# Kernel tuning notes

Hardware: AMD Instinct MI355X
Metric: run time of the kernel (lower is better)

The kernel has to match this reference:

```python
import jax, jax.numpy as jnp
import numpy as np

N_WORDS, L, VOCAB, D = 8192, 24, 128, 512
H, DK = 8, 64  # n_head, d_v (=d_k)
N_NAMES, WORDS_PER_NAME = 2048, 4
N_CONCEPTS, NAMES_PER_CONCEPT = 256, 8


def setup_inputs() -> dict:
    key = jax.random.key(0)
    ks = jax.random.split(key, 9)
    s = 1.0 / np.sqrt(D).astype(np.float32)
    inputs = jax.random.randint(ks[0], (N_WORDS, L), 0, VOCAB)  # 0 = pad char
    n_words = jnp.full((N_NAMES,), WORDS_PER_NAME, dtype=jnp.int32)
    n_names = jnp.full((N_CONCEPTS,), NAMES_PER_CONCEPT, dtype=jnp.int32)
    return {
        "inputs": inputs,
        "n_words": n_words,
        "n_names": n_names,
        "emb": jax.random.normal(ks[1], (VOCAB, D), jnp.float32) * s,
        "Wq": jax.random.normal(ks[2], (D, H * DK), jnp.float32) * s,
        "Wk": jax.random.normal(ks[3], (D, H * DK), jnp.float32) * s,
        "Wv": jax.random.normal(ks[4], (D, H * DK), jnp.float32) * s,
        "Wo": jax.random.normal(ks[5], (H * DK, D), jnp.float32) * s,
        "W1": jax.random.normal(ks[6], (D, 512), jnp.float32) * s,
        "W2": jax.random.normal(ks[7], (512, 256), jnp.float32) * s,
    }


def reference(inputs, n_words, n_names, emb, Wq, Wk, Wv, Wo, W1, W2):
    N, Lq = inputs.shape
    pad = inputs == 0  # [N, L] padding mask (char id 0)

    # --- MHAEncoder: embedding + masked multi-head self-attention ---
    x = emb[inputs]  # [N, L, D]
    def split_heads(t):  # [N, L, H*DK] -> [N, H, L, DK]
        return t.reshape(N, Lq, H, DK).transpose(0, 2, 1, 3)
    q = split_heads(x @ Wq)
    k = split_heads(x @ Wk)
    v = split_heads(x @ Wv)
    scale = jnp.asarray(1.0 / np.sqrt(DK), x.dtype)
    scores = jnp.einsum('nhqd,nhkd->nhqk', q, k) * scale  # [N, H, L, L]
    scores = jnp.where(pad[:, None, None, :], jnp.asarray(-1e9, x.dtype), scores)
    attn = jax.nn.softmax(scores, axis=-1)
    o = jnp.einsum('nhqk,nhkd->nhqd', attn, v)
    word_ft = o.transpose(0, 2, 1, 3).reshape(N, Lq, H * DK) @ Wo  # [N, L, D]

    # --- masked mean pooling over chars: matmul(mask, word_ft)/mask.sum(-1) ---
    m = (~pad).astype(word_ft.dtype)  # [N, L]
    name_emb = jnp.einsum('nl,nld->nd', m, word_ft) / m.sum(-1, keepdims=True)  # [N, D]

    # --- split(n_words) + per-group mean == segment mean over word groups ---
    G = n_words.shape[0]
    seg = jnp.repeat(jnp.arange(G), n_words, total_repeat_length=N)
    name_ft = jax.ops.segment_sum(name_emb, seg, num_segments=G)
    name_ft = name_ft / n_words[:, None].astype(name_ft.dtype)  # [G, D]

    # --- small no-bias Tanh MLP ---
    h = jnp.tanh(name_ft @ W1)
    out = jnp.tanh(h @ W2)  # [G, 256]
    # final .split(n_names) is a view-only regrouping; return the packed array
    return out
```

## Files before the change

kernel.cpp:

```cpp
#include <hip/hip_runtime.h>
#include <math.h>

#define NWORDS 8192
#define LW     24
#define VOC    128
#define DIM    512
#define NH     8
#define DKH    64
#define GNAMES 2048
#define F2     256

#define S1_LEN 458752

#define GEMM_BODY(A_, B_, K_, N_, m0_, n0_, kbeg_, kchunk_)                         \
  __shared__ float As[2][16][68];                                                   \
  __shared__ float Bs[2][16][68];                                                   \
  const int t = threadIdx.x, tx = t & 15, ty = t >> 4;                              \
  float acc[4][4] = {};                                                             \
  float ra[4], rb[4];                                                               \
  _Pragma("unroll")                                                                 \
  for (int i = 0; i < 4; ++i) { int idx = t + 256 * i;                              \
    ra[i] = A_[(size_t)(m0_ + (idx >> 4)) * K_ + kbeg_ + (idx & 15)]; }             \
  _Pragma("unroll")                                                                 \
  for (int i = 0; i < 4; ++i) { int idx = t + 256 * i;                              \
    rb[i] = B_[(size_t)(kbeg_ + (idx >> 6)) * N_ + n0_ + (idx & 63)]; }             \
  _Pragma("unroll")                                                                 \
  for (int i = 0; i < 4; ++i) { int idx = t + 256 * i; As[0][idx & 15][idx >> 4] = ra[i]; } \
  _Pragma("unroll")                                                                 \
  for (int i = 0; i < 4; ++i) { int idx = t + 256 * i; Bs[0][idx >> 6][idx & 63] = rb[i]; } \
  __syncthreads();                                                                  \
  int buf = 0;                                                                      \
  for (int k0 = kbeg_; k0 < kbeg_ + kchunk_; k0 += 16) {                            \
    const bool more = (k0 + 16 < kbeg_ + kchunk_);                                  \
    if (more) {                                                                     \
      _Pragma("unroll")                                                             \
      for (int i = 0; i < 4; ++i) { int idx = t + 256 * i;                          \
        ra[i] = A_[(size_t)(m0_ + (idx >> 4)) * K_ + (k0 + 16) + (idx & 15)]; }     \
      _Pragma("unroll")                                                             \
      for (int i = 0; i < 4; ++i) { int idx = t + 256 * i;                          \
        rb[i] = B_[(size_t)(k0 + 16 + (idx >> 6)) * N_ + n0_ + (idx & 63)]; }       \
    }                                                                               \
    _Pragma("unroll")                                                               \
    for (int k = 0; k < 16; ++k) {                                                  \
      float a[4], b[4];                                                             \
      _Pragma("unroll")                                                             \
      for (int i = 0; i < 4; ++i) a[i] = As[buf][k][ty * 4 + i];                    \
      _Pragma("unroll")                                                             \
      for (int j = 0; j < 4; ++j) b[j] = Bs[buf][k][tx * 4 + j];                    \
      _Pragma("unroll")                                                             \
      for (int i = 0; i < 4; ++i)                                                   \
        _Pragma("unroll")                                                           \
        for (int j = 0; j < 4; ++j) acc[i][j] += a[i] * b[j];                       \
    }                                                                               \
    if (more) {                                                                     \
      _Pragma("unroll")                                                             \
      for (int i = 0; i < 4; ++i) { int idx = t + 256 * i; As[buf ^ 1][idx & 15][idx >> 4] = ra[i]; } \
      _Pragma("unroll")                                                             \
      for (int i = 0; i < 4; ++i) { int idx = t + 256 * i; Bs[buf ^ 1][idx >> 6][idx & 63] = rb[i]; } \
      __syncthreads();                                                              \
      buf ^= 1;                                                                     \
    }                                                                               \
  }

template<int NSPLIT>
__global__ __launch_bounds__(256) void k_stage1(const float* __restrict__ emb,
                                                const float* __restrict__ Wq,
                                                const float* __restrict__ Wk,
                                                const float* __restrict__ Wv,
                                                const float* __restrict__ Wo,
                                                const float* __restrict__ W1,
                                                float* __restrict__ P) {
  const int tid = blockIdx.x, s = blockIdx.y;
  const float *A, *B;
  int coff, m0, n0;
  if (tid < 48) {
    const int g = tid >> 4, mt = tid & 15;
    A = emb;
    B = (g == 0) ? Wq : ((g == 1) ? Wk : Wv);
    coff = g * 65536;
    m0 = (mt >> 3) * 64; n0 = (mt & 7) * 64;
  } else {
    const int id = tid - 48;
    A = Wo; B = W1; coff = 3 * 65536;
    m0 = (id >> 3) * 64; n0 = (id & 7) * 64;
  }
  const int kchunk = 512 / NSPLIT, kbeg = s * kchunk;
  GEMM_BODY(A, B, 512, 512, m0, n0, kbeg, kchunk)
  float* Cp = P + (size_t)s * S1_LEN + coff;
  #pragma unroll
  for (int i = 0; i < 4; ++i) {
    float4 v = make_float4(acc[i][0], acc[i][1], acc[i][2], acc[i][3]);
    *(float4*)&Cp[(size_t)(m0 + ty * 4 + i) * 512 + n0 + tx * 4] = v;
  }
}

__global__ __launch_bounds__(256) void k_gemm_ilv(const float* __restrict__ A,
                                                  const float* __restrict__ B,
                                                  float* __restrict__ P,
                                                  int kchunk) {
  const int m0 = blockIdx.y * 64, n0 = blockIdx.x * 64;
  const int kbeg = blockIdx.z * kchunk;
  const int sz = blockIdx.z;
  GEMM_BODY(A, B, 512, 512, m0, n0, kbeg, kchunk)
  float4* P4 = (float4*)P;
  #pragma unroll
  for (int i = 0; i < 4; ++i) {
    float4 v = make_float4(acc[i][0], acc[i][1], acc[i][2], acc[i][3]);
    P4[((size_t)(m0 + ty * 4 + i) * 128 + (n0 >> 2) + tx) * 4 + sz] = v;
  }
}

__global__ __launch_bounds__(256) void k_npool(const float* __restrict__ Wn,
                                               const float* __restrict__ EV,
                                               float* __restrict__ NP) {
  const int m0 = blockIdx.x * 64, h = blockIdx.y;
  const float* A2 = Wn + (size_t)m0 * 1024 + h * 128;
  const float* B2 = EV + h * 64;
  GEMM_BODY(A2, B2, 1024, 512, 0, 0, 0, 128)
  #pragma unroll
  for (int i = 0; i < 4; ++i) {
    float4 v = make_float4(acc[i][0], acc[i][1], acc[i][2], acc[i][3]);
    *(float4*)&NP[(size_t)(m0 + ty * 4 + i) * 512 + h * 64 + tx * 4] = v;
  }
}

__global__ __launch_bounds__(256) void k_gemm_tail(const float* __restrict__ P,
                                                   const float* __restrict__ B,
                                                   float* __restrict__ C,
                                                   int kchunk) {
  const int N = 256, K = 512;
  __shared__ float As[2][16][68];
  __shared__ float Bs[2][16][68];
  const int t = threadIdx.x, tx = t & 15, ty = t >> 4;
  const int m0 = blockIdx.y * 64, n0 = blockIdx.x * 64;
  const int kbeg = blockIdx.z * kchunk;
  const float4* P4 = (const float4*)P;
  const int am = t >> 2, ak = t & 3;
  float acc[4][4] = {};
  float4 ta;
  float rb[4];
#define TAIL_LOAD_A(kb)                                                   \
  {                                                                       \
    size_t b4 = ((size_t)(m0 + am) * 128 + ((kb) >> 2) + ak) * 4;         \
    float4 p0 = P4[b4 + 0], p1 = P4[b4 + 1], p2 = P4[b4 + 2], p3 = P4[b4 + 3]; \
    ta.x = tanhf(p0.x + p1.x + p2.x + p3.x);                              \
    ta.y = tanhf(p0.y + p1.y + p2.y + p3.y);                              \
    ta.z = tanhf(p0.z + p1.z + p2.z + p3.z);                              \
    ta.w = tanhf(p0.w + p1.w + p2.w + p3.w);                              \
  }
#define TAIL_LOAD_B(kb)                                                   \
  _Pragma("unroll")                                                       \
  for (int i = 0; i < 4; ++i) { int idx = t + 256 * i;                    \
    rb[i] = B[(size_t)((kb) + (idx >> 6)) * N + n0 + (idx & 63)]; }
#define TAIL_STORE(bb)                                                    \
  { int kk = ak * 4;                                                      \
    As[bb][kk + 0][am] = ta.x; As[bb][kk + 1][am] = ta.y;                 \
    As[bb][kk + 2][am] = ta.z; As[bb][kk + 3][am] = ta.w; }               \
  _Pragma("unroll")                                                       \
  for (int i = 0; i < 4; ++i) { int idx = t + 256 * i;                    \
    Bs[bb][idx >> 6][idx & 63] = rb[i]; }
  TAIL_LOAD_A(kbeg)
  TAIL_LOAD_B(kbeg)
  TAIL_STORE(0)
  __syncthreads();
  int buf = 0;
  for (int k0 = kbeg; k0 < kbeg + kchunk; k0 += 16) {
    const bool more = (k0 + 16 < kbeg + kchunk);
    if (more) { TAIL_LOAD_A(k0 + 16) TAIL_LOAD_B(k0 + 16) }
    #pragma unroll
    for (int k = 0; k < 16; ++k) {
      float a[4], b[4];
      #pragma unroll
      for (int i = 0; i < 4; ++i) a[i] = As[buf][k][ty * 4 + i];
      #pragma unroll
      for (int j = 0; j < 4; ++j) b[j] = Bs[buf][k][tx * 4 + j];
      #pragma unroll
      for (int i = 0; i < 4; ++i)
        #pragma unroll
        for (int j = 0; j < 4; ++j) acc[i][j] += a[i] * b[j];
    }
    if (more) { TAIL_STORE(buf ^ 1) __syncthreads(); buf ^= 1; }
  }
  float* Cp = C + (size_t)blockIdx.z * (GNAMES * F2);
  #pragma unroll
  for (int i = 0; i < 4; ++i) {
    float4 v = make_float4(acc[i][0], acc[i][1], acc[i][2], acc[i][3]);
    *(float4*)&Cp[(size_t)(m0 + ty * 4 + i) * N + n0 + tx * 4] = v;
  }
}

template<int ACT, int S>
__global__ __launch_bounds__(256) void k_reduce(const float* __restrict__ P,
                                                float* __restrict__ O,
                                                int len4, int stride4) {
  const int i = blockIdx.x * 256 + threadIdx.x;
  if (i >= len4) return;
  const float4* P4 = (const float4*)P;
  float4 a = P4[i];
  #pragma unroll
  for (int s = 1; s < S; ++s) {
    float4 b = P4[(size_t)s * stride4 + i];
    a.x += b.x; a.y += b.y; a.z += b.z; a.w += b.w;
  }
  if (ACT) { a.x = tanhf(a.x); a.y = tanhf(a.y); a.z = tanhf(a.z); a.w = tanhf(a.w); }
  ((float4*)O)[i] = a;
}

__global__ __launch_bounds__(128) void k_qk_tab(const float* __restrict__ EQ,
                                                const float* __restrict__ EK,
                                                float* __restrict__ etab) {
  const int c1 = blockIdx.x, h = blockIdx.y, c2 = threadIdx.x;
  __shared__ float qrow[DKH];
  if (threadIdx.x < DKH) qrow[threadIdx.x] = EQ[c1 * DIM + h * DKH + threadIdx.x];
  __syncthreads();
  const float* krow = EK + c2 * DIM + h * DKH;
  float acc = 0.f;
  #pragma unroll
  for (int d = 0; d < DKH; ++d) acc += qrow[d] * krow[d];
  float e = (c1 != 0 && c2 != 0) ? __expf(acc * 0.125f) : 0.f;
  etab[((size_t)c1 * VOC + c2) * NH + h] = e;
}

__global__ __launch_bounds__(256) void k_bins(const int* __restrict__ inputs,
                                              const int* __restrict__ nwords,
                                              const float* __restrict__ etab,
                                              float* __restrict__ Wn) {
  const int g = blockIdx.x, t = threadIdx.x;
  const int wv = t >> 6, l = t & 63;
  const int h = l & 7, qg = l >> 3;
  __shared__ float bins[VOC * NH];
  __shared__ int wred[4];
  __shared__ int sh_nwg;

  for (int i = t; i < VOC * NH; i += 256) bins[i] = 0.f;
  int partial = 0;
  for (int i = t; i < GNAMES; i += 256) {
    int v = nwords[i];
    partial += (i < g) ? v : 0;
    if (i == g) sh_nwg = v;
  }
  #pragma unroll
  for (int d = 1; d < 64; d <<= 1) partial += __shfl_xor(partial, d);
  if (l == 0) wred[wv] = partial;
  __syncthreads();
  const int nw = sh_nwg;
  const int o0 = wred[0] + wred[1] + wred[2] + wred[3];

  for (int wrel = wv; wrel < nw; wrel += 4) {
    const int wi = o0 + wrel;
    int c_l = (l < LW) ? inputs[(size_t)wi * LW + l] : 0;
    unsigned long long mk = __ballot(c_l != 0);
    int cnt = __popcll(mk);
    float invc = cnt ? 1.f / (float)cnt : 0.f;

    int cq0 = __shfl(c_l, qg);
    int cq1 = __shfl(c_l, qg + 8);
    int cq2 = __shfl(c_l, qg + 16);
    const float* b0 = etab + (cq0 << 10) + h;
    const float* b1 = etab + (cq1 << 10) + h;
    const float* b2 = etab + (cq2 << 10) + h;

    float r0[LW], r1[LW], r2[LW];
    float d0 = 0.f, d1 = 0.f, d2 = 0.f;
    #pragma unroll
    for (int kp = 0; kp < LW; ++kp) {
      int o = __shfl(c_l, kp) << 3;
      r0[kp] = b0[o]; r1[kp] = b1[o]; r2[kp] = b2[o];
      d0 += r0[kp]; d1 += r1[kp]; d2 += r2[kp];
    }
    float i0 = cq0 ? invc / d0 : 0.f;
    float i1 = cq1 ? invc / d1 : 0.f;
    float i2 = cq2 ? invc / d2 : 0.f;

    #pragma unroll
    for (int kp = 0; kp < LW; ++kp) {
      int ck = __shfl(c_l, kp);
      if (ck) {
        float v = r0[kp] * i0 + r1[kp] * i1 + r2[kp] * i2;
        v += __shfl_xor(v, 8);
        v += __shfl_xor(v, 16);
        v += __shfl_xor(v, 32);
        if (qg == 0) atomicAdd(&bins[(ck << 3) + h], v);
      }
    }
  }
  __syncthreads();

  const float invn = nw ? 1.f / (float)nw : 0.f;
  for (int i = t; i < NH * VOC; i += 256) {
    int hh = i >> 7, cc = i & 127;
    Wn[(size_t)g * 1024 + i] = bins[(cc << 3) + hh] * invn;
  }
}

extern "C" void kernel_launch(void* const* d_in, const int* in_sizes, int n_in,
                              void* d_out, int out_size, void* d_ws, size_t ws_size,
                              hipStream_t stream) {
  const int*   inputs  = (const int*)d_in[0];
  const int*   n_words = (const int*)d_in[1];
  const float* emb     = (const float*)d_in[3];
  const float* Wq      = (const float*)d_in[4];
  const float* Wk      = (const float*)d_in[5];
  const float* Wv      = (const float*)d_in[6];
  const float* Wo      = (const float*)d_in[7];
  const float* W1      = (const float*)d_in[8];
  const float* W2      = (const float*)d_in[9];
  float* out = (float*)d_out;

  float* ws   = (float*)d_ws;
  float* ES   = ws;
  float* BIG  = ws + 458752;
  float* TAB  = ws + 4653056;
  float* NP   = ws + 4784128;
  float* Wn   = ws + 5832704;
  float* OUTP = ws + 7929856;

  k_stage1<4><<<dim3(112, 4), 256, 0, stream>>>(emb, Wq, Wk, Wv, Wo, W1, BIG);
  k_reduce<0, 4><<<S1_LEN / 4 / 256, 256, 0, stream>>>(BIG, ES, S1_LEN / 4, S1_LEN / 4);
  k_qk_tab<<<dim3(VOC, NH), 128, 0, stream>>>(ES, ES + 65536, TAB);
  k_bins<<<GNAMES, 256, 0, stream>>>(inputs, n_words, TAB, Wn);
  k_npool<<<dim3(GNAMES / 64, NH), 256, 0, stream>>>(Wn, ES + 131072, NP);
  k_gemm_ilv<<<dim3(8, 32, 4), 256, 0, stream>>>(NP, ES + 196608, BIG, 128);
  k_gemm_tail<<<dim3(4, 32, 4), 256, 0, stream>>>(BIG, W2, OUTP, 128);
  k_reduce<1, 4><<<(GNAMES * F2) / 4 / 256, 256, 0, stream>>>(OUTP, out, (GNAMES * F2) / 4, (GNAMES * F2) / 4);
}
```

Before: 105.7 us.

## Drop split-K in tail GEMM with fused tanh; stage bins scores in fp16 LDS

```diff
diff --git a/kernel.cpp b/kernel.cpp
--- a/kernel.cpp
+++ b/kernel.cpp
@@ -1,4 +1,5 @@
 #include <hip/hip_runtime.h>
+#include <hip/hip_fp16.h>
 #include <math.h>
 
 #define NWORDS 8192
@@ -126,14 +127,12 @@
 
 __global__ __launch_bounds__(256) void k_gemm_tail(const float* __restrict__ P,
                                                    const float* __restrict__ B,
-                                                   float* __restrict__ C,
-                                                   int kchunk) {
+                                                   float* __restrict__ C) {
   const int N = 256, K = 512;
   __shared__ float As[2][16][68];
   __shared__ float Bs[2][16][68];
   const int t = threadIdx.x, tx = t & 15, ty = t >> 4;
   const int m0 = blockIdx.y * 64, n0 = blockIdx.x * 64;
-  const int kbeg = blockIdx.z * kchunk;
   const float4* P4 = (const float4*)P;
   const int am = t >> 2, ak = t & 3;
   float acc[4][4] = {};
@@ -159,13 +158,13 @@
   _Pragma("unroll")                                                       \
   for (int i = 0; i < 4; ++i) { int idx = t + 256 * i;                    \
     Bs[bb][idx >> 6][idx & 63] = rb[i]; }
-  TAIL_LOAD_A(kbeg)
-  TAIL_LOAD_B(kbeg)
+  TAIL_LOAD_A(0)
+  TAIL_LOAD_B(0)
   TAIL_STORE(0)
   __syncthreads();
   int buf = 0;
-  for (int k0 = kbeg; k0 < kbeg + kchunk; k0 += 16) {
-    const bool more = (k0 + 16 < kbeg + kchunk);
+  for (int k0 = 0; k0 < K; k0 += 16) {
+    const bool more = (k0 + 16 < K);
     if (more) { TAIL_LOAD_A(k0 + 16) TAIL_LOAD_B(k0 + 16) }
     #pragma unroll
     for (int k = 0; k < 16; ++k) {
@@ -181,11 +180,11 @@
     }
     if (more) { TAIL_STORE(buf ^ 1) __syncthreads(); buf ^= 1; }
   }
-  float* Cp = C + (size_t)blockIdx.z * (GNAMES * F2);
   #pragma unroll
   for (int i = 0; i < 4; ++i) {
-    float4 v = make_float4(acc[i][0], acc[i][1], acc[i][2], acc[i][3]);
-    *(float4*)&Cp[(size_t)(m0 + ty * 4 + i) * N + n0 + tx * 4] = v;
+    float4 v = make_float4(tanhf(acc[i][0]), tanhf(acc[i][1]),
+                           tanhf(acc[i][2]), tanhf(acc[i][3]));
+    *(float4*)&C[(size_t)(m0 + ty * 4 + i) * N + n0 + tx * 4] = v;
   }
 }
 
@@ -228,23 +227,25 @@
   const int g = blockIdx.x, t = threadIdx.x;
   const int wv = t >> 6, l = t & 63;
   const int h = l & 7, qg = l >> 3;
+  __shared__ __half sc[4][LW][3][64];
   __shared__ float bins[VOC * NH];
-  __shared__ int wred[4];
-  __shared__ int sh_nwg;
-
-  for (int i = t; i < VOC * NH; i += 256) bins[i] = 0.f;
+
+  int* iscr = (int*)bins;
   int partial = 0;
   for (int i = t; i < GNAMES; i += 256) {
     int v = nwords[i];
     partial += (i < g) ? v : 0;
-    if (i == g) sh_nwg = v;
+    if (i == g) iscr[4] = v;
   }
   #pragma unroll
   for (int d = 1; d < 64; d <<= 1) partial += __shfl_xor(partial, d);
-  if (l == 0) wred[wv] = partial;
-  __syncthreads();
-  const int nw = sh_nwg;
-  const int o0 = wred[0] + wred[1] + wred[2] + wred[3];
+  if (l == 0) iscr[wv] = partial;
+  __syncthreads();
+  const int nw = iscr[4];
+  const int o0 = iscr[0] + iscr[1] + iscr[2] + iscr[3];
+  __syncthreads();
+  for (int i = t; i < VOC * NH; i += 256) bins[i] = 0.f;
+  __syncthreads();
 
   for (int wrel = wv; wrel < nw; wrel += 4) {
     const int wi = o0 + wrel;
@@ -260,13 +261,15 @@
     const float* b1 = etab + (cq1 << 10) + h;
     const float* b2 = etab + (cq2 << 10) + h;
 
-    float r0[LW], r1[LW], r2[LW];
     float d0 = 0.f, d1 = 0.f, d2 = 0.f;
     #pragma unroll
     for (int kp = 0; kp < LW; ++kp) {
       int o = __shfl(c_l, kp) << 3;
-      r0[kp] = b0[o]; r1[kp] = b1[o]; r2[kp] = b2[o];
-      d0 += r0[kp]; d1 += r1[kp]; d2 += r2[kp];
+      float e0 = b0[o], e1 = b1[o], e2 = b2[o];
+      d0 += e0; d1 += e1; d2 += e2;
+      sc[wv][kp][0][l] = __float2half(e0);
+      sc[wv][kp][1][l] = __float2half(e1);
+      sc[wv][kp][2][l] = __float2half(e2);
     }
     float i0 = cq0 ? invc / d0 : 0.f;
     float i1 = cq1 ? invc / d1 : 0.f;
@@ -276,7 +279,9 @@
     for (int kp = 0; kp < LW; ++kp) {
       int ck = __shfl(c_l, kp);
       if (ck) {
-        float v = r0[kp] * i0 + r1[kp] * i1 + r2[kp] * i2;
+        float v = __half2float(sc[wv][kp][0][l]) * i0
+                + __half2float(sc[wv][kp][1][l]) * i1
+                + __half2float(sc[wv][kp][2][l]) * i2;
         v += __shfl_xor(v, 8);
         v += __shfl_xor(v, 16);
         v += __shfl_xor(v, 32);
@@ -313,7 +318,7 @@
   float* TAB  = ws + 4653056;
   float* NP   = ws + 4784128;
   float* Wn   = ws + 5832704;
-  float* OUTP = ws + 7929856;
+  int*  UNUSED = (int*)(ws + 7929856);
 
   k_stage1<4><<<dim3(112, 4), 256, 0, stream>>>(emb, Wq, Wk, Wv, Wo, W1, BIG);
   k_reduce<0, 4><<<S1_LEN / 4 / 256, 256, 0, stream>>>(BIG, ES, S1_LEN / 4, S1_LEN / 4);
@@ -321,6 +326,5 @@
   k_bins<<<GNAMES, 256, 0, stream>>>(inputs, n_words, TAB, Wn);
   k_npool<<<dim3(GNAMES / 64, NH), 256, 0, stream>>>(Wn, ES + 131072, NP);
   k_gemm_ilv<<<dim3(8, 32, 4), 256, 0, stream>>>(NP, ES + 196608, BIG, 128);
-  k_gemm_tail<<<dim3(4, 32, 4), 256, 0, stream>>>(BIG, W2, OUTP, 128);
-  k_reduce<1, 4><<<(GNAMES * F2) / 4 / 256, 256, 0, stream>>>(OUTP, out, (GNAMES * F2) / 4, (GNAMES * F2) / 4);
-}
+  k_gemm_tail<<<dim3(4, 32, 1), 256, 0, stream>>>(BIG, W2, out);
+}
```

After: 138.3 us. 1.31x slower.

## Fold split-K reduce into QK table and precompute EV·W per head

Applied to the files above, without the earlier changes.

```diff
diff --git a/kernel.cpp b/kernel.cpp
--- a/kernel.cpp
+++ b/kernel.cpp
@@ -94,6 +94,84 @@
   }
 }
 
+__global__ __launch_bounds__(256) void k_tab_evw(const float* __restrict__ P,
+                                                 float* __restrict__ etab,
+                                                 float* __restrict__ EVW) {
+  __shared__ float As[64][65];
+  __shared__ float Bs[64][65];
+  const int t = threadIdx.x, tx = t & 15, ty = t >> 4;
+  const int b = blockIdx.x;
+
+  if (b < 32) {
+    const int h = b >> 2, mt = (b >> 1) & 1, nt = b & 1;
+    const int m0 = mt * 64, n0 = nt * 64;
+    #pragma unroll
+    for (int i = 0; i < 16; ++i) {
+      int idx = t + 256 * i;
+      int r = idx >> 6, d = idx & 63;
+      size_t ao = (size_t)(m0 + r) * 512 + h * 64 + d;
+      As[d][r] = P[ao] + P[ao + S1_LEN] + P[ao + 2 * S1_LEN] + P[ao + 3 * S1_LEN];
+      size_t bo = 65536 + (size_t)(n0 + r) * 512 + h * 64 + d;
+      Bs[d][r] = P[bo] + P[bo + S1_LEN] + P[bo + 2 * S1_LEN] + P[bo + 3 * S1_LEN];
+    }
+    __syncthreads();
+    float acc[4][4] = {};
+    for (int d = 0; d < 64; ++d) {
+      float a[4], bb[4];
+      #pragma unroll
+      for (int i = 0; i < 4; ++i) a[i] = As[d][ty * 4 + i];
+      #pragma unroll
+      for (int j = 0; j < 4; ++j) bb[j] = Bs[d][tx * 4 + j];
+      #pragma unroll
+      for (int i = 0; i < 4; ++i)
+        #pragma unroll
+        for (int j = 0; j < 4; ++j) acc[i][j] += a[i] * bb[j];
+    }
+    #pragma unroll
+    for (int i = 0; i < 4; ++i) {
+      int c1 = m0 + ty * 4 + i;
+      #pragma unroll
+      for (int j = 0; j < 4; ++j) {
+        int c2 = n0 + tx * 4 + j;
+        float e = (c1 != 0 && c2 != 0) ? __expf(acc[i][j] * 0.125f) : 0.f;
+        etab[((size_t)c1 * VOC + c2) * NH + h] = e;
+      }
+    }
+  } else {
+    const int b2 = b - 32;
+    const int h = b2 >> 4, mt = (b2 >> 3) & 1, nt = b2 & 7;
+    const int m0 = mt * 64, n0 = nt * 64;
+    #pragma unroll
+    for (int i = 0; i < 16; ++i) {
+      int idx = t + 256 * i;
+      int r = idx >> 6, d = idx & 63;
+      size_t ao = 131072 + (size_t)(m0 + r) * 512 + h * 64 + d;
+      As[d][r] = P[ao] + P[ao + S1_LEN] + P[ao + 2 * S1_LEN] + P[ao + 3 * S1_LEN];
+      size_t bo = 196608 + (size_t)(h * 64 + r) * 512 + n0 + d;
+      Bs[r][d] = P[bo] + P[bo + S1_LEN] + P[bo + 2 * S1_LEN] + P[bo + 3 * S1_LEN];
+    }
+    __syncthreads();
+    float acc[4][4] = {};
+    for (int d = 0; d < 64; ++d) {
+      float a[4], bb[4];
+      #pragma unroll
+      for (int i = 0; i < 4; ++i) a[i] = As[d][ty * 4 + i];
+      #pragma unroll
+      for (int j = 0; j < 4; ++j) bb[j] = Bs[d][tx * 4 + j];
+      #pragma unroll
+      for (int i = 0; i < 4; ++i)
+        #pragma unroll
+        for (int j = 0; j < 4; ++j) acc[i][j] += a[i] * bb[j];
+    }
+    #pragma unroll
+    for (int i = 0; i < 4; ++i) {
+      int cg = m0 + ty * 4 + i;
+      float4 v = make_float4(acc[i][0], acc[i][1], acc[i][2], acc[i][3]);
+      *(float4*)&EVW[(size_t)(h * 128 + cg) * 512 + n0 + tx * 4] = v;
+    }
+  }
+}
+
 __global__ __launch_bounds__(256) void k_gemm_ilv(const float* __restrict__ A,
                                                   const float* __restrict__ B,
                                                   float* __restrict__ P,
@@ -101,26 +179,12 @@
   const int m0 = blockIdx.y * 64, n0 = blockIdx.x * 64;
   const int kbeg = blockIdx.z * kchunk;
   const int sz = blockIdx.z;
-  GEMM_BODY(A, B, 512, 512, m0, n0, kbeg, kchunk)
+  GEMM_BODY(A, B, 1024, 512, m0, n0, kbeg, kchunk)
   float4* P4 = (float4*)P;
   #pragma unroll
   for (int i = 0; i < 4; ++i) {
     float4 v = make_float4(acc[i][0], acc[i][1], acc[i][2], acc[i][3]);
-    P4[((size_t)(m0 + ty * 4 + i) * 128 + (n0 >> 2) + tx) * 4 + sz] = v;
-  }
-}
-
-__global__ __launch_bounds__(256) void k_npool(const float* __restrict__ Wn,
-                                               const float* __restrict__ EV,
-                                               float* __restrict__ NP) {
-  const int m0 = blockIdx.x * 64, h = blockIdx.y;
-  const float* A2 = Wn + (size_t)m0 * 1024 + h * 128;
-  const float* B2 = EV + h * 64;
-  GEMM_BODY(A2, B2, 1024, 512, 0, 0, 0, 128)
-  #pragma unroll
-  for (int i = 0; i < 4; ++i) {
-    float4 v = make_float4(acc[i][0], acc[i][1], acc[i][2], acc[i][3]);
-    *(float4*)&NP[(size_t)(m0 + ty * 4 + i) * 512 + h * 64 + tx * 4] = v;
+    P4[((size_t)(m0 + ty * 4 + i) * 128 + (n0 >> 2) + tx) * 8 + sz] = v;
   }
 }
 
@@ -141,12 +205,13 @@
   float rb[4];
 #define TAIL_LOAD_A(kb)                                                   \
   {                                                                       \
-    size_t b4 = ((size_t)(m0 + am) * 128 + ((kb) >> 2) + ak) * 4;         \
+    size_t b4 = ((size_t)(m0 + am) * 128 + ((kb) >> 2) + ak) * 8;         \
     float4 p0 = P4[b4 + 0], p1 = P4[b4 + 1], p2 = P4[b4 + 2], p3 = P4[b4 + 3]; \
-    ta.x = tanhf(p0.x + p1.x + p2.x + p3.x);                              \
-    ta.y = tanhf(p0.y + p1.y + p2.y + p3.y);                              \
-    ta.z = tanhf(p0.z + p1.z + p2.z + p3.z);                              \
-    ta.w = tanhf(p0.w + p1.w + p2.w + p3.w);                              \
+    float4 p4 = P4[b4 + 4], p5 = P4[b4 + 5], p6 = P4[b4 + 6], p7 = P4[b4 + 7]; \
+    ta.x = tanhf(p0.x + p1.x + p2.x + p3.x + p4.x + p5.x + p6.x + p7.x);  \
+    ta.y = tanhf(p0.y + p1.y + p2.y + p3.y + p4.y + p5.y + p6.y + p7.y);  \
+    ta.z = tanhf(p0.z + p1.z + p2.z + p3.z + p4.z + p5.z + p6.z + p7.z);  \
+    ta.w = tanhf(p0.w + p1.w + p2.w + p3.w + p4.w + p5.w + p6.w + p7.w);  \
   }
 #define TAIL_LOAD_B(kb)                                                   \
   _Pragma("unroll")                                                       \
@@ -206,21 +271,6 @@
   ((float4*)O)[i] = a;
 }
 
-__global__ __launch_bounds__(128) void k_qk_tab(const float* __restrict__ EQ,
-                                                const float* __restrict__ EK,
-                                                float* __restrict__ etab) {
-  const int c1 = blockIdx.x, h = blockIdx.y, c2 = threadIdx.x;
-  __shared__ float qrow[DKH];
-  if (threadIdx.x < DKH) qrow[threadIdx.x] = EQ[c1 * DIM + h * DKH + threadIdx.x];
-  __syncthreads();
-  const float* krow = EK + c2 * DIM + h * DKH;
-  float acc = 0.f;
-  #pragma unroll
-  for (int d = 0; d < DKH; ++d) acc += qrow[d] * krow[d];
-  float e = (c1 != 0 && c2 != 0) ? __expf(acc * 0.125f) : 0.f;
-  etab[((size_t)c1 * VOC + c2) * NH + h] = e;
-}
-
 __global__ __launch_bounds__(256) void k_bins(const int* __restrict__ inputs,
                                               const int* __restrict__ nwords,
                                               const float* __restrict__ etab,
@@ -308,19 +358,17 @@
   float* out = (float*)d_out;
 
   float* ws   = (float*)d_ws;
-  float* ES   = ws;
-  float* BIG  = ws + 458752;
-  float* TAB  = ws + 4653056;
-  float* NP   = ws + 4784128;
-  float* Wn   = ws + 5832704;
-  float* OUTP = ws + 7929856;
+  float* BIG  = ws;
+  float* TAB  = ws + 1835008;
+  float* EVW  = ws + 1966080;
+  float* Wn   = ws + 2490368;
+  float* ILVP = ws + 4587520;
+  float* OUTP = ws + 12976128;
 
   k_stage1<4><<<dim3(112, 4), 256, 0, stream>>>(emb, Wq, Wk, Wv, Wo, W1, BIG);
-  k_reduce<0, 4><<<S1_LEN / 4 / 256, 256, 0, stream>>>(BIG, ES, S1_LEN / 4, S1_LEN / 4);
-  k_qk_tab<<<dim3(VOC, NH), 128, 0, stream>>>(ES, ES + 65536, TAB);
+  k_tab_evw<<<160, 256, 0, stream>>>(BIG, TAB, EVW);
   k_bins<<<GNAMES, 256, 0, stream>>>(inputs, n_words, TAB, Wn);
-  k_npool<<<dim3(GNAMES / 64, NH), 256, 0, stream>>>(Wn, ES + 131072, NP);
-  k_gemm_ilv<<<dim3(8, 32, 4), 256, 0, stream>>>(NP, ES + 196608, BIG, 128);
-  k_gemm_tail<<<dim3(4, 32, 4), 256, 0, stream>>>(BIG, W2, OUTP, 128);
+  k_gemm_ilv<<<dim3(8, 32, 8), 256, 0, stream>>>(Wn, EVW, ILVP, 128);
+  k_gemm_tail<<<dim3(4, 32, 4), 256, 0, stream>>>(ILVP, W2, OUTP, 128);
   k_reduce<1, 4><<<(GNAMES * F2) / 4 / 256, 256, 0, stream>>>(OUTP, out, (GNAMES * F2) / 4, (GNAMES * F2) / 4);
 }
```

After: 130.3 us. +23.2%, slower.
